# Optimization experiments

Measured on AMD Instinct MI355X. Metric: run time of the kernel, lower is better.

The kernel has to match this reference:

```python
import jax, jax.numpy as jnp
import numpy as np

M = 8192            # number of graphs (m)
NODES_PER_GRAPH = 64
N = M * NODES_PER_GRAPH  # total nodes (n)
D_H = 128
D_X = 128


def setup_inputs() -> dict:
    key = jax.random.key(0)
    k1, k2, k3 = jax.random.split(key, 3)
    # scale by 0.1 so the unstabilized exp(e) in segment_softmax stays finite in fp32
    h = 0.1 * jax.random.normal(k1, (M, D_H), dtype=jnp.float32)
    x = 0.1 * jax.random.normal(k2, (N, D_X), dtype=jnp.float32)
    a = jax.random.uniform(k3, (D_H, D_X), dtype=jnp.float32)  # th.rand init
    batch_num_nodes = jnp.full((M,), NODES_PER_GRAPH, dtype=jnp.int32)
    return {"h": h, "x": x, "a": a, "batch_num_nodes": batch_num_nodes}


def reference(h, x, a, batch_num_nodes):
    m = batch_num_nodes.shape[0]
    n = x.shape[0]
    # node -> graph segment ids (repeat_interleave of arange)
    seg = jnp.repeat(jnp.arange(m), batch_num_nodes, total_repeat_length=n)  # (n,)
    ha = (h @ a)[seg]                       # (n, d_x): gather per-graph query to nodes
    e = jnp.sum(x * ha, axis=1)             # (n,) attention logits
    ex = jnp.exp(e)                         # unstabilized exp, faithful to source
    z = jax.ops.segment_sum(ex, seg, num_segments=m)   # (m,) partition functions
    att = ex / z[seg]                       # (n,) segment softmax
    out = jax.ops.segment_sum(att[:, None] * x, seg, num_segments=m)  # (m, d_x)
    return out
```

## Files before the change

kernel.cpp:

```cpp
#include <hip/hip_runtime.h>


#define NPG  64
#define DDIM 128
#define SROW 132

typedef __attribute__((ext_vector_type(4))) float f32x4;

__global__ __launch_bounds__(256) void gat_softmax_kernel(
    const float* __restrict__ h,
    const float* __restrict__ x,
    const float* __restrict__ a,
    float* __restrict__ out)
{
    const int g = blockIdx.x;
    const int t = threadIdx.x;

    __shared__ __align__(16) float xs[NPG * SROW];
    __shared__ float hq[DDIM];
    __shared__ float qpart[2][DDIM];
    __shared__ float q[DDIM];
    __shared__ __align__(16) float epart[256];
    __shared__ float att[NPG];
    __shared__ float opart[2][DDIM];

    const f32x4* xg = reinterpret_cast<const f32x4*>(x + (size_t)g * (NPG * DDIM));
    #pragma unroll
    for (int it = 0; it < 8; ++it) {
        int c = it * 256 + t;
        f32x4 v = xg[c];
        int row = c >> 5;
        int col = c & 31;
        *reinterpret_cast<f32x4*>(&xs[row * SROW + col * 4]) = v;
    }
    if (t < DDIM) hq[t] = h[(size_t)g * DDIM + t];
    __syncthreads();

    {
        const int j    = t & (DDIM - 1);
        const int half = t >> 7;
        const float* ap = a + (size_t)(half * 64) * DDIM + j;
        float acc = 0.f;
        #pragma unroll 16
        for (int k = 0; k < 64; ++k)
            acc += hq[half * 64 + k] * ap[(size_t)k * DDIM];
        qpart[half][j] = acc;
    }
    __syncthreads();
    if (t < DDIM) q[t] = qpart[0][t] + qpart[1][t];
    __syncthreads();

    {
        const int i       = t >> 2;
        const int quarter = t & 3;
        const float* xrow = &xs[i * SROW + quarter * 32];
        const float* qq   = &q[quarter * 32];
        float acc = 0.f;
        #pragma unroll
        for (int c = 0; c < 8; ++c) {
            f32x4 v = *reinterpret_cast<const f32x4*>(xrow + c * 4);
            acc += v[0] * qq[c*4] + v[1] * qq[c*4+1] + v[2] * qq[c*4+2] + v[3] * qq[c*4+3];
        }
        epart[t] = acc;
    }
    __syncthreads();

    if (t < NPG) {
        f32x4 p = *reinterpret_cast<const f32x4*>(&epart[4 * t]);
        float e  = p[0] + p[1] + p[2] + p[3];
        float ex = expf(e);
        float z  = ex;
        #pragma unroll
        for (int m = 32; m >= 1; m >>= 1)
            z += __shfl_xor(z, m, 64);
        att[t] = ex / z;
    }
    __syncthreads();

    {
        const int j   = t & (DDIM - 1);
        const int grp = t >> 7;
        float acc = 0.f;
        #pragma unroll
        for (int k = 0; k < 32; ++k) {
            int i = grp * 32 + k;
            acc += att[i] * xs[i * SROW + j];
        }
        opart[grp][j] = acc;
    }
    __syncthreads();

    if (t < DDIM)
        out[(size_t)g * DDIM + t] = opart[0][t] + opart[1][t];
}

extern "C" void kernel_launch(void* const* d_in, const int* in_sizes, int n_in,
                              void* d_out, int out_size, void* d_ws, size_t ws_size,
                              hipStream_t stream) {
    const float* h = (const float*)d_in[0];
    const float* x = (const float*)d_in[1];
    const float* a = (const float*)d_in[2];
    float* out = (float*)d_out;

    const int m = in_sizes[0] / DDIM;
    gat_softmax_kernel<<<m, 256, 0, stream>>>(h, x, a, out);
}
```

Baseline: 372.1 us.

## Split h@a into a separate batched GEMM kernel and streamline attention kernel

Computes h@a in a dedicated kernel where each block handles 8 graph rows, so each load of a is reused across four rows instead of every block re-reading all of a. The attention kernel then reads its precomputed query vector from workspace into registers. It also cuts barriers by reducing logits and partition sums with wave shuffles, and uses vectorized weighted accumulation over 8 node groups. The costs are an extra kernel launch and a workspace round trip for ha, plus a fast __expf approximation.

```diff
diff --git a/kernel.cpp b/kernel.cpp
--- a/kernel.cpp
+++ b/kernel.cpp
@@ -7,91 +7,104 @@
 
 typedef __attribute__((ext_vector_type(4))) float f32x4;
 
-__global__ __launch_bounds__(256) void gat_softmax_kernel(
-    const float* __restrict__ h,
-    const float* __restrict__ x,
-    const float* __restrict__ a,
-    float* __restrict__ out)
+__global__ __launch_bounds__(256) void ha_gemm_kernel(
+    const float* __restrict__ h, const float* __restrict__ a, float* __restrict__ ha)
+{
+    const int j    = threadIdx.x & 127;
+    const int rg   = threadIdx.x >> 7;
+    const int row0 = blockIdx.x * 8 + rg * 4;
+    const float* hp = h + (size_t)row0 * DDIM;
+
+    float acc0 = 0.f, acc1 = 0.f, acc2 = 0.f, acc3 = 0.f;
+    #pragma unroll 8
+    for (int k4 = 0; k4 < 32; ++k4) {
+        f32x4 h0 = *(const f32x4*)(hp + 0 * DDIM + k4 * 4);
+        f32x4 h1 = *(const f32x4*)(hp + 1 * DDIM + k4 * 4);
+        f32x4 h2 = *(const f32x4*)(hp + 2 * DDIM + k4 * 4);
+        f32x4 h3 = *(const f32x4*)(hp + 3 * DDIM + k4 * 4);
+        #pragma unroll
+        for (int kk = 0; kk < 4; ++kk) {
+            float av = a[(k4 * 4 + kk) * DDIM + j];
+            acc0 += h0[kk] * av;
+            acc1 += h1[kk] * av;
+            acc2 += h2[kk] * av;
+            acc3 += h3[kk] * av;
+        }
+    }
+    float* op = ha + (size_t)row0 * DDIM + j;
+    op[0 * DDIM] = acc0; op[1 * DDIM] = acc1; op[2 * DDIM] = acc2; op[3 * DDIM] = acc3;
+}
+
+__global__ __launch_bounds__(256) void attn_kernel(
+    const float* __restrict__ x, const float* __restrict__ ha, float* __restrict__ out)
 {
     const int g = blockIdx.x;
     const int t = threadIdx.x;
 
     __shared__ __align__(16) float xs[NPG * SROW];
-    __shared__ float hq[DDIM];
-    __shared__ float qpart[2][DDIM];
-    __shared__ float q[DDIM];
-    __shared__ __align__(16) float epart[256];
-    __shared__ float att[NPG];
-    __shared__ float opart[2][DDIM];
+    __shared__ float exbuf[NPG];
+    __shared__ float zbuf[4];
+    __shared__ __align__(16) float opart[8][DDIM];
 
-    const f32x4* xg = reinterpret_cast<const f32x4*>(x + (size_t)g * (NPG * DDIM));
+    const int qt = t & 3;
+    const int i  = t >> 2;
+    f32x4 qv[8];
+    const float* qp = ha + (size_t)g * DDIM + qt * 32;
+    #pragma unroll
+    for (int c = 0; c < 8; ++c) qv[c] = *(const f32x4*)(qp + c * 4);
+
+    const f32x4* xg = (const f32x4*)(x + (size_t)g * (NPG * DDIM));
     #pragma unroll
     for (int it = 0; it < 8; ++it) {
         int c = it * 256 + t;
         f32x4 v = xg[c];
-        int row = c >> 5;
-        int col = c & 31;
-        *reinterpret_cast<f32x4*>(&xs[row * SROW + col * 4]) = v;
-    }
-    if (t < DDIM) hq[t] = h[(size_t)g * DDIM + t];
-    __syncthreads();
-
-    {
-        const int j    = t & (DDIM - 1);
-        const int half = t >> 7;
-        const float* ap = a + (size_t)(half * 64) * DDIM + j;
-        float acc = 0.f;
-        #pragma unroll 16
-        for (int k = 0; k < 64; ++k)
-            acc += hq[half * 64 + k] * ap[(size_t)k * DDIM];
-        qpart[half][j] = acc;
-    }
-    __syncthreads();
-    if (t < DDIM) q[t] = qpart[0][t] + qpart[1][t];
-    __syncthreads();
-
-    {
-        const int i       = t >> 2;
-        const int quarter = t & 3;
-        const float* xrow = &xs[i * SROW + quarter * 32];
-        const float* qq   = &q[quarter * 32];
-        float acc = 0.f;
-        #pragma unroll
-        for (int c = 0; c < 8; ++c) {
-            f32x4 v = *reinterpret_cast<const f32x4*>(xrow + c * 4);
-            acc += v[0] * qq[c*4] + v[1] * qq[c*4+1] + v[2] * qq[c*4+2] + v[3] * qq[c*4+3];
-        }
-        epart[t] = acc;
+        int row = c >> 5, col = c & 31;
+        *(f32x4*)(&xs[row * SROW + col * 4]) = v;
     }
     __syncthreads();
 
-    if (t < NPG) {
-        f32x4 p = *reinterpret_cast<const f32x4*>(&epart[4 * t]);
-        float e  = p[0] + p[1] + p[2] + p[3];
-        float ex = expf(e);
-        float z  = ex;
+    const float* xrow = &xs[i * SROW + qt * 32];
+    float acc = 0.f;
+    #pragma unroll
+    for (int c = 0; c < 8; ++c) {
+        f32x4 v = *(const f32x4*)(xrow + c * 4);
+        acc += v[0] * qv[c][0] + v[1] * qv[c][1] + v[2] * qv[c][2] + v[3] * qv[c][3];
+    }
+    acc += __shfl_xor(acc, 1, 64);
+    acc += __shfl_xor(acc, 2, 64);
+    float ex = __expf(acc);
+    float zw = ex;
+    zw += __shfl_xor(zw, 4, 64);
+    zw += __shfl_xor(zw, 8, 64);
+    zw += __shfl_xor(zw, 16, 64);
+    zw += __shfl_xor(zw, 32, 64);
+    if (qt == 0)       exbuf[i] = ex;
+    if ((t & 63) == 0) zbuf[t >> 6] = zw;
+    __syncthreads();
+
+    const float rz = 1.0f / (zbuf[0] + zbuf[1] + zbuf[2] + zbuf[3]);
+
+    {
+        const int jb  = (t & 31) * 4;
+        const int grp = t >> 5;
+        f32x4 o = {0.f, 0.f, 0.f, 0.f};
         #pragma unroll
-        for (int m = 32; m >= 1; m >>= 1)
-            z += __shfl_xor(z, m, 64);
-        att[t] = ex / z;
+        for (int k = 0; k < 8; ++k) {
+            int node = grp * 8 + k;
+            float w = exbuf[node] * rz;
+            f32x4 v = *(const f32x4*)(&xs[node * SROW + jb]);
+            o[0] += w * v[0]; o[1] += w * v[1]; o[2] += w * v[2]; o[3] += w * v[3];
+        }
+        *(f32x4*)(&opart[grp][jb]) = o;
     }
     __syncthreads();
 
-    {
-        const int j   = t & (DDIM - 1);
-        const int grp = t >> 7;
-        float acc = 0.f;
+    if (t < DDIM) {
+        float o = 0.f;
         #pragma unroll
-        for (int k = 0; k < 32; ++k) {
-            int i = grp * 32 + k;
-            acc += att[i] * xs[i * SROW + j];
-        }
-        opart[grp][j] = acc;
+        for (int gq = 0; gq < 8; ++gq) o += opart[gq][t];
+        out[(size_t)g * DDIM + t] = o;
     }
-    __syncthreads();
-
-    if (t < DDIM)
-        out[(size_t)g * DDIM + t] = opart[0][t] + opart[1][t];
 }
 
 extern "C" void kernel_launch(void* const* d_in, const int* in_sizes, int n_in,
@@ -101,7 +114,9 @@
     const float* x = (const float*)d_in[1];
     const float* a = (const float*)d_in[2];
     float* out = (float*)d_out;
+    float* ha  = (float*)d_ws;
 
     const int m = in_sizes[0] / DDIM;
-    gat_softmax_kernel<<<m, 256, 0, stream>>>(h, x, a, out);
+    ha_gemm_kernel<<<m / 8, 256, 0, stream>>>(h, a, ha);
+    attn_kernel<<<m, 256, 0, stream>>>(x, ha, out);
 }
```

After: 386.3 us. 1.04x slower.
